# Kernel tuning notes

Measured on AMD Instinct MI355X. Metric: run time of the kernel, lower is better.

## Reference

```python
import jax, jax.numpy as jnp
import numpy as np

N, E = 20000, 160000
H, C1, C_OUT, D_IN = 4, 256, 512, 128
HID = H * C1  # 1024


def gat_conv(x, src, dst, W, a_src, a_dst, b, heads, ch, concat):
    n = x.shape[0]
    xw = (x @ W).reshape(n, heads, ch)                     # [N,H,C]
    es = jnp.sum(xw * a_src, axis=-1)                      # [N,H]
    ed = jnp.sum(xw * a_dst, axis=-1)                      # [N,H]
    e = jax.nn.leaky_relu(es[src] + ed[dst], 0.2)          # [Etot,H]
    m = jax.ops.segment_max(e, dst, num_segments=n)
    m = jnp.where(jnp.isfinite(m), m, 0.0)
    p = jnp.exp(e - m[dst])
    denom = jax.ops.segment_sum(p, dst, num_segments=n)
    alpha = p / (denom[dst] + 1e-16)                       # segment softmax
    out = jax.ops.segment_sum(alpha[:, :, None] * xw[src], dst, num_segments=n)
    out = out.reshape(n, heads * ch) if concat else out.mean(axis=1)
    return out + b


def layer_norm(x, g, b, eps=1e-5):
    mu = jnp.mean(x, axis=-1, keepdims=True)
    var = jnp.var(x, axis=-1, keepdims=True)
    return (x - mu) * jax.lax.rsqrt(var + eps) * g + b


def setup_inputs() -> dict:
    key = jax.random.key(0)
    ks = jax.random.split(key, 16)
    s1, s2, s3 = (2.0 / D_IN) ** 0.5, (2.0 / HID) ** 0.5, (2.0 / HID) ** 0.5
    return {
        "x": jax.random.normal(ks[0], (N, D_IN), jnp.float32),
        "edge_index": jax.random.randint(ks[1], (2, E), 0, N, jnp.int64),
        "W1": jax.random.normal(ks[2], (D_IN, H * C1), jnp.float32) * s1,
        "a_src1": jax.random.normal(ks[3], (H, C1), jnp.float32) * 0.1,
        "a_dst1": jax.random.normal(ks[4], (H, C1), jnp.float32) * 0.1,
        "b1": jnp.zeros((HID,), jnp.float32),
        "ln1_g": jnp.ones((HID,), jnp.float32),
        "ln1_b": jnp.zeros((HID,), jnp.float32),
        "W2": jax.random.normal(ks[5], (HID, H * C1), jnp.float32) * s2,
        "a_src2": jax.random.normal(ks[6], (H, C1), jnp.float32) * 0.1,
        "a_dst2": jax.random.normal(ks[7], (H, C1), jnp.float32) * 0.1,
        "b2": jnp.zeros((HID,), jnp.float32),
        "ln2_g": jnp.ones((HID,), jnp.float32),
        "ln2_b": jnp.zeros((HID,), jnp.float32),
        "W3": jax.random.normal(ks[8], (HID, C_OUT), jnp.float32) * s3,
        "a_src3": jax.random.normal(ks[9], (1, C_OUT), jnp.float32) * 0.1,
        "a_dst3": jax.random.normal(ks[10], (1, C_OUT), jnp.float32) * 0.1,
        "b3": jnp.zeros((C_OUT,), jnp.float32),
    }


def reference(x, edge_index, W1, a_src1, a_dst1, b1, ln1_g, ln1_b,
              W2, a_src2, a_dst2, b2, ln2_g, ln2_b,
              W3, a_src3, a_dst3, b3):
    # add self loops (PyG GATConv default add_self_loops=True)
    loops = jnp.arange(N, dtype=edge_index.dtype)
    src = jnp.concatenate([edge_index[0], loops])
    dst = jnp.concatenate([edge_index[1], loops])

    h = gat_conv(x, src, dst, W1, a_src1, a_dst1, b1, H, C1, True)
    h = jax.nn.elu(layer_norm(h, ln1_g, ln1_b))  # dropout: eval mode (identity)
    h = gat_conv(h, src, dst, W2, a_src2, a_dst2, b2, H, C1, True)
    h = jax.nn.elu(layer_norm(h, ln2_g, ln2_b))
    out = gat_conv(h, src, dst, W3, a_src3, a_dst3, b3, 1, C_OUT, True)
    return out
```

## Files before the change

kernel.cpp:

```cpp
#include <hip/hip_runtime.h>
#include <hip/hip_bf16.h>

typedef __hip_bfloat16 bf16;
typedef __attribute__((ext_vector_type(8))) short short8;
typedef __attribute__((ext_vector_type(4))) float float4v;

#define NN 20000
#define EE 160000
#define ET (NN + EE)

__device__ __forceinline__ float bf2f(bf16 v){ return __bfloat162float(v); }
__device__ __forceinline__ float raw2f(unsigned short u){ return __uint_as_float(((unsigned)u) << 16); }

struct Ptrs { const void* p[18]; int n[18]; };

__global__ void k_detect(Ptrs P, int* __restrict__ flags){
  int b = blockIdx.x;
  int t = threadIdx.x;
  if (b == 1){
    const int* e = (const int*)P.p[1];
    int odd = e[2*t + 1];
    unsigned long long m2 = __ballot(odd != 0);
    if (t == 0){ flags[1] = (m2 == 0ULL) ? 1 : 0; }
    return;
  }
  const unsigned* w = (const unsigned*)P.p[b];
  int nwords = P.n[b] / 2;
  unsigned v = w[t % nwords];
  int e8 = (v >> 7) & 0xFF;
  int looks = (e8 >= 100 && e8 <= 140) ? 1 : 0;
  unsigned long long mz = __ballot(v == 0u);
  unsigned long long ml = __ballot(looks);
  if (t == 0){
    int nz = __popcll(mz);
    int nonz = 64 - nz;
    int nl = __popcll(ml);
    flags[8+b] = (nonz > 0 && 2*nl >= nonz) ? 0 : 1;
  }
}

struct P13 { const void* src[13]; int off[13]; int n[13]; int fi[13]; };
struct PrepArgs {
  const void* xraw; bf16* Xc;
  const void* w1raw; bf16* Wt1;
  const void* w2raw; bf16* Wt2;
  const void* w3raw; bf16* Wt3;
  const int* eiraw; int* eic;
  P13 p13; float* prm;
  int* counts;
  const int* flags;
};

__device__ __forceinline__ void do_transpose(float (*tile)[33], const void* raw,
    bf16* wt, int K, int M, int f, int bx, int by, int t){
  int kb = by*32, mb = bx*32;
  int tx = t & 31, ty = t >> 5;
  for (int r = 0; r < 4; r++){
    int k = kb + ty + r*8;
    int m = mb + tx;
    float v = f ? ((const float*)raw)[(size_t)k*M+m] : bf2f(((const bf16*)raw)[(size_t)k*M+m]);
    tile[ty + r*8][tx] = v;
  }
  __syncthreads();
  for (int r = 0; r < 4; r++){
    int m = mb + ty + r*8;
    int k = kb + tx;
    wt[(size_t)m*K + k] = __float2bfloat16(tile[tx][ty + r*8]);
  }
}

__global__ __launch_bounds__(256) void k_prep(PrepArgs A){
  __shared__ float tile[32][33];
  int b = blockIdx.x, t = threadIdx.x;
  const int* flags = A.flags;
  if (b < 10000){
    int i = b*256 + t;
    if (flags[8+0]) A.Xc[i] = __float2bfloat16(((const float*)A.xraw)[i]);
    else            A.Xc[i] = ((const bf16*)A.xraw)[i];
  } else if (b < 10128){
    int r = b - 10000;
    do_transpose(tile, A.w1raw, A.Wt1, 128, 1024, flags[8+2], r & 31, r >> 5, t);
  } else if (b < 11152){
    int r = b - 10128;
    do_transpose(tile, A.w2raw, A.Wt2, 1024, 1024, flags[8+8], r & 31, r >> 5, t);
  } else if (b < 11664){
    int r = b - 11152;
    do_transpose(tile, A.w3raw, A.Wt3, 1024, 512, flags[8+14], r & 15, r >> 4, t);
  } else if (b < 12914){
    int i = (b - 11664)*256 + t;
    if (i < 2*EE) A.eic[i] = flags[1] ? A.eiraw[2*i] : A.eiraw[i];
  } else if (b < 12927){
    int pb = b - 12914;
    const void* s = A.p13.src[pb];
    int n = A.p13.n[pb];
    float* d = A.prm + A.p13.off[pb];
    int f = flags[8 + A.p13.fi[pb]];
    for (int i = t; i < n; i += 256)
      d[i] = f ? ((const float*)s)[i] : bf2f(((const bf16*)s)[i]);
  } else {
    int i = (b - 12927)*256 + t;
    if (i < NN) A.counts[i] = 1;
  }
}

__global__ void k_hist(const int* __restrict__ ei, int* __restrict__ counts){
  int e = blockIdx.x*256 + threadIdx.x;
  if (e < EE){
    int d = ei[EE + e];
    if (d >= 0 && d < NN) atomicAdd(&counts[d], 1);
  }
}

__global__ __launch_bounds__(1024) void k_scan(const int* __restrict__ counts, int* __restrict__ rp){
  __shared__ int wsum[16];
  __shared__ int sc;
  int t = threadIdx.x, lane = t & 63, wv = t >> 6;
  if (t == 0) sc = 0;
  __syncthreads();
  for (int base = 0; base < NN; base += 1024){
    int i = base + t;
    int v = (i < NN) ? counts[i] : 0;
    int x = v;
    #pragma unroll
    for (int o = 1; o < 64; o <<= 1){
      int y = __shfl_up(x, o, 64);
      if (lane >= o) x += y;
    }
    if (lane == 63) wsum[wv] = x;
    __syncthreads();
    if (wv == 0 && lane < 16){
      int w = wsum[lane];
      #pragma unroll
      for (int o = 1; o < 16; o <<= 1){
        int y = __shfl_up(w, o, 16);
        if ((lane & 15) >= o) w += y;
      }
      wsum[lane] = w;
    }
    __syncthreads();
    int carry = sc;
    int wpre = (wv > 0) ? wsum[wv-1] : 0;
    if (i < NN) rp[i] = carry + wpre + x - v;
    __syncthreads();
    if (t == 1023) sc = carry + wsum[15];
    __syncthreads();
  }
  if (t == 0) rp[NN] = sc;
}

__global__ void k_selfloop(const int* __restrict__ rp, int* __restrict__ cursor, int* __restrict__ col){
  int i = blockIdx.x*256 + threadIdx.x;
  if (i < NN){ int p = rp[i]; col[p] = i; cursor[i] = p + 1; }
}

__global__ void k_scatter(const int* __restrict__ ei, int* __restrict__ cursor, int* __restrict__ col){
  int e = blockIdx.x*256 + threadIdx.x;
  if (e < EE){
    int s = ei[e], d = ei[EE + e];
    if (d >= 0 && d < NN){
      int pos = atomicAdd(&cursor[d], 1);
      col[pos] = s;
    }
  }
}

__global__ void k_zero2(float* __restrict__ a, float* __restrict__ b, int n){
  int i = blockIdx.x*256 + threadIdx.x;
  if (i < n){ a[i] = 0.f; b[i] = 0.f; }
}

__global__ __launch_bounds__(256) void k_gemm_mfma(
    const bf16* __restrict__ X, const bf16* __restrict__ Wt, bf16* __restrict__ Y,
    const float* __restrict__ as_, const float* __restrict__ ad_,
    float* __restrict__ es, float* __restrict__ ed,
    int K, int M, int C, int H)
{
  __shared__ bf16 Xs[128*32];
  __shared__ bf16 Bs[128*32];
  int tid  = threadIdx.x;
  int wave = tid >> 6, lane = tid & 63;
  int quad = lane >> 4, l15 = lane & 15;
  int c0 = blockIdx.x * 128;
  int r0 = blockIdx.y * 128;
  int wr = (wave >> 1) * 64;
  int wc = (wave & 1) * 64;

  float4v acc[4][4];
  #pragma unroll
  for (int i=0;i<4;i++)
    #pragma unroll
    for (int j=0;j<4;j++)
      acc[i][j] = (float4v){0.f,0.f,0.f,0.f};

  for (int k0 = 0; k0 < K; k0 += 32){
    #pragma unroll
    for (int i = 0; i < 2; i++){
      int ch = i*256 + tid;
      int row = ch >> 2, kp = ch & 3;
      const bf16* gx = X  + (size_t)(r0 + row)*K + k0 + kp*8;
      const bf16* gb = Wt + (size_t)(c0 + row)*K + k0 + kp*8;
      __builtin_amdgcn_global_load_lds(
        (const __attribute__((address_space(1))) unsigned int*)gx,
        (__attribute__((address_space(3))) unsigned int*)(Xs + ch*8), 16, 0, 0);
      __builtin_amdgcn_global_load_lds(
        (const __attribute__((address_space(1))) unsigned int*)gb,
        (__attribute__((address_space(3))) unsigned int*)(Bs + ch*8), 16, 0, 0);
    }
    __syncthreads();

    short8 af[4], bfr[4];
    #pragma unroll
    for (int i = 0; i < 4; i++)
      af[i]  = *(const short8*)(Xs + ((size_t)(wr + i*16 + l15))*32 + quad*8);
    #pragma unroll
    for (int j = 0; j < 4; j++)
      bfr[j] = *(const short8*)(Bs + ((size_t)(wc + j*16 + l15))*32 + quad*8);
    #pragma unroll
    for (int i = 0; i < 4; i++)
      #pragma unroll
      for (int j = 0; j < 4; j++)
        acc[i][j] = __builtin_amdgcn_mfma_f32_16x16x32_bf16(af[i], bfr[j], acc[i][j], 0, 0, 0);
    __syncthreads();
  }

  int h = c0 / C;
  float asv[4], adv[4];
  #pragma unroll
  for (int j = 0; j < 4; j++){
    int colj = c0 + wc + j*16 + l15;
    asv[j] = as_[colj]; adv[j] = ad_[colj];
  }
  #pragma unroll
  for (int i = 0; i < 4; i++){
    int rbase = r0 + wr + i*16 + quad*4;
    #pragma unroll
    for (int rg = 0; rg < 4; rg++){
      int row = rbase + rg;
      bool ok = (row < NN);
      float pe = 0.f, pd = 0.f;
      #pragma unroll
      for (int j = 0; j < 4; j++){
        float v = acc[i][j][rg];
        int colj = c0 + wc + j*16 + l15;
        if (ok) Y[(size_t)row*M + colj] = __float2bfloat16(v);
        pe += v * asv[j];
        pd += v * adv[j];
      }
      #pragma unroll
      for (int o = 1; o < 16; o <<= 1){
        pe += __shfl_xor(pe, o, 64);
        pd += __shfl_xor(pd, o, 64);
      }
      if (ok && l15 == 0){
        atomicAdd(&es[row*H + h], pe);
        atomicAdd(&ed[row*H + h], pd);
      }
    }
  }
}

#define DCAP 1024
__global__ __launch_bounds__(256) void k_aggln(const int* __restrict__ rp, const int* __restrict__ col,
    const bf16* __restrict__ xw, const float* __restrict__ es, const float* __restrict__ ed,
    const float* __restrict__ bias, const float* __restrict__ gam, const float* __restrict__ bet,
    bf16* __restrict__ act){
  int n = blockIdx.x, t = threadIdx.x;
  int h = t >> 6;
  __shared__ float llog[DCAP][4];
  __shared__ int ssrc[DCAP];
  __shared__ float smv[4], srd[4];
  __shared__ float ls1[256], ls2[256];
  int e0 = rp[n], e1 = rp[n+1], deg = e1 - e0;
  float4 ed4 = *(const float4*)&ed[n*4];
  float a0=0.f, a1=0.f, a2=0.f, a3=0.f;

  if (deg <= DCAP){
    for (int j = t; j < deg; j += 256){
      int s = col[e0 + j];
      ssrc[j] = s;
      float4 e4 = *(const float4*)&es[s*4];
      float v0 = e4.x + ed4.x; llog[j][0] = v0 > 0.f ? v0 : 0.2f*v0;
      float v1 = e4.y + ed4.y; llog[j][1] = v1 > 0.f ? v1 : 0.2f*v1;
      float v2 = e4.z + ed4.z; llog[j][2] = v2 > 0.f ? v2 : 0.2f*v2;
      float v3 = e4.w + ed4.w; llog[j][3] = v3 > 0.f ? v3 : 0.2f*v3;
    }
    __syncthreads();
    if (t < 4){
      float m = -1e30f;
      for (int j = 0; j < deg; j++) m = fmaxf(m, llog[j][t]);
      float den = 0.f;
      for (int j = 0; j < deg; j++) den += __expf(llog[j][t] - m);
      smv[t] = m; srd[t] = 1.f/(den + 1e-16f);
    }
    __syncthreads();
    for (int j = t; j < deg; j += 256){
      #pragma unroll
      for (int hh = 0; hh < 4; hh++)
        llog[j][hh] = __expf(llog[j][hh] - smv[hh]) * srd[hh];
    }
    __syncthreads();
    for (int j = 0; j < deg; j++){
      int s = ssrc[j];
      float al = llog[j][h];
      ushort4 u = *(const ushort4*)((const unsigned short*)xw + (size_t)s*1024 + 4*t);
      a0 += al * raw2f(u.x);
      a1 += al * raw2f(u.y);
      a2 += al * raw2f(u.z);
      a3 += al * raw2f(u.w);
    }
  } else {
    if (t < 4){
      float m = -1e30f;
      for (int e = e0; e < e1; e++){
        float v = es[col[e]*4 + t] + ed[n*4 + t];
        v = v > 0.f ? v : 0.2f*v;
        m = fmaxf(m, v);
      }
      float den = 0.f;
      for (int e = e0; e < e1; e++){
        float v = es[col[e]*4 + t] + ed[n*4 + t];
        v = v > 0.f ? v : 0.2f*v;
        den += __expf(v - m);
      }
      smv[t] = m; srd[t] = 1.f/(den + 1e-16f);
    }
    __syncthreads();
    float edh = ed[n*4 + h];
    for (int e = e0; e < e1; e++){
      int s = col[e];
      float v = es[s*4 + h] + edh;
      v = v > 0.f ? v : 0.2f*v;
      float al = __expf(v - smv[h]) * srd[h];
      ushort4 u = *(const ushort4*)((const unsigned short*)xw + (size_t)s*1024 + 4*t);
      a0 += al * raw2f(u.x);
      a1 += al * raw2f(u.y);
      a2 += al * raw2f(u.z);
      a3 += al * raw2f(u.w);
    }
  }

  a0 += bias[4*t+0]; a1 += bias[4*t+1]; a2 += bias[4*t+2]; a3 += bias[4*t+3];
  float s1 = a0+a1+a2+a3;
  float s2 = a0*a0+a1*a1+a2*a2+a3*a3;
  ls1[t] = s1; ls2[t] = s2;
  __syncthreads();
  for (int o = 128; o > 0; o >>= 1){
    if (t < o){ ls1[t] += ls1[t+o]; ls2[t] += ls2[t+o]; }
    __syncthreads();
  }
  float mu  = ls1[0] * (1.f/1024.f);
  float var = ls2[0] * (1.f/1024.f) - mu*mu;
  float rstd = rsqrtf(fmaxf(var, 0.f) + 1e-5f);
  float v0 = (a0-mu)*rstd*gam[4*t+0] + bet[4*t+0];
  float v1 = (a1-mu)*rstd*gam[4*t+1] + bet[4*t+1];
  float v2 = (a2-mu)*rstd*gam[4*t+2] + bet[4*t+2];
  float v3 = (a3-mu)*rstd*gam[4*t+3] + bet[4*t+3];
  v0 = v0 > 0.f ? v0 : (__expf(v0)-1.f);
  v1 = v1 > 0.f ? v1 : (__expf(v1)-1.f);
  v2 = v2 > 0.f ? v2 : (__expf(v2)-1.f);
  v3 = v3 > 0.f ? v3 : (__expf(v3)-1.f);
  ushort4 o4;
  { bf16 hh2=__float2bfloat16(v0); o4.x=*(unsigned short*)&hh2; }
  { bf16 hh2=__float2bfloat16(v1); o4.y=*(unsigned short*)&hh2; }
  { bf16 hh2=__float2bfloat16(v2); o4.z=*(unsigned short*)&hh2; }
  { bf16 hh2=__float2bfloat16(v3); o4.w=*(unsigned short*)&hh2; }
  *(ushort4*)((unsigned short*)act + (size_t)n*1024 + 4*t) = o4;
}

__global__ __launch_bounds__(256) void k_agg3(const int* __restrict__ rp, const int* __restrict__ col,
    const bf16* __restrict__ xw, const float* __restrict__ es, const float* __restrict__ ed,
    const float* __restrict__ bias, float* __restrict__ out){
  int n = blockIdx.x, t = threadIdx.x;
  __shared__ float llog[DCAP];
  __shared__ int ssrc[DCAP];
  __shared__ float smv, srd;
  int e0 = rp[n], e1 = rp[n+1], deg = e1 - e0;
  float edv = ed[n];
  float a0 = 0.f, a1 = 0.f;

  if (deg <= DCAP){
    for (int j = t; j < deg; j += 256){
      int s = col[e0 + j];
      ssrc[j] = s;
      float v = es[s] + edv;
      llog[j] = v > 0.f ? v : 0.2f*v;
    }
    __syncthreads();
    if (t == 0){
      float m = -1e30f;
      for (int j = 0; j < deg; j++) m = fmaxf(m, llog[j]);
      float den = 0.f;
      for (int j = 0; j < deg; j++) den += __expf(llog[j] - m);
      smv = m; srd = 1.f/(den + 1e-16f);
    }
    __syncthreads();
    for (int j = t; j < deg; j += 256)
      llog[j] = __expf(llog[j] - smv) * srd;
    __syncthreads();
    for (int j = 0; j < deg; j++){
      int s = ssrc[j];
      float al = llog[j];
      ushort2 u = *(const ushort2*)((const unsigned short*)xw + (size_t)s*512 + 2*t);
      a0 += al * raw2f(u.x);
      a1 += al * raw2f(u.y);
    }
  } else {
    if (t == 0){
      float m = -1e30f;
      for (int e = e0; e < e1; e++){
        float v = es[col[e]] + edv;
        v = v > 0.f ? v : 0.2f*v;
        m = fmaxf(m, v);
      }
      float den = 0.f;
      for (int e = e0; e < e1; e++){
        float v = es[col[e]] + edv;
        v = v > 0.f ? v : 0.2f*v;
        den += __expf(v - m);
      }
      smv = m; srd = 1.f/(den + 1e-16f);
    }
    __syncthreads();
    for (int e = e0; e < e1; e++){
      int s = col[e];
      float v = es[s] + edv;
      v = v > 0.f ? v : 0.2f*v;
      float al = __expf(v - smv) * srd;
      ushort2 u = *(const ushort2*)((const unsigned short*)xw + (size_t)s*512 + 2*t);
      a0 += al * raw2f(u.x);
      a1 += al * raw2f(u.y);
    }
  }
  out[(size_t)n*512 + 2*t]     = a0 + bias[2*t];
  out[(size_t)n*512 + 2*t + 1] = a1 + bias[2*t+1];
}

__global__ void k_wssmall(float* __restrict__ out, float code){
  if (threadIdx.x == 0) out[0] = code;
}

extern "C" void kernel_launch(void* const* d_in, const int* in_sizes, int n_in,
                              void* d_out, int out_size, void* d_ws, size_t ws_size,
                              hipStream_t stream){
  float* out = (float*)d_out;
  char* ws = (char*)d_ws;

  static const int EXP_SZ[18] = {2560000, 320000, 131072, 1024,1024,1024,1024,1024,
                                 1048576, 1024,1024,1024,1024,1024,
                                 524288, 512,512,512};
  if (n_in != 18){ k_wssmall<<<1,64,0,stream>>>(out, 500.0f*301.0f); return; }
  for (int i = 0; i < 18; i++)
    if (in_sizes[i] != EXP_SZ[i]){ k_wssmall<<<1,64,0,stream>>>(out, 500.0f*302.0f); return; }
  if (out_size != NN*512){ k_wssmall<<<1,64,0,stream>>>(out, 500.0f*303.0f); return; }
  const size_t NEED = 93215360;
  if (ws_size < NEED){ k_wssmall<<<1,64,0,stream>>>(out, 500.0f*304.0f); return; }

  bf16* xw    = (bf16*) (ws);
  bf16* act   = (bf16*) (ws + 40960000);
  bf16* Xc    = (bf16*) (ws + 81920000);
  bf16* Wt1   = (bf16*) (ws + 87040000);
  bf16* Wt2   = (bf16*) (ws + 87302144);
  bf16* Wt3   = (bf16*) (ws + 89399296);
  float* prm  = (float*)(ws + 90447872);
  int*  flags = (int*)  (ws + 90494976);
  int*  eic   = (int*)  (ws + 90495232);
  float* es   = (float*)(ws + 91775232);
  int*  cur   = (int*)  (ws + 91775232);
  float* ed   = (float*)(ws + 92095232);
  int*  rp    = (int*)  (ws + 92415232);
  int*  col   = (int*)  (ws + 92495360);

  float *as1=prm+0, *ad1=prm+1024, *b1=prm+2048, *lg1=prm+3072, *lb1=prm+4096;
  float *as2=prm+5120, *ad2=prm+6144, *b2=prm+7168, *lg2=prm+8192, *lb2=prm+9216;
  float *as3=prm+10240, *ad3=prm+10752, *b3=prm+11264;

  const int TB = 256;
  int gbN = (NN + TB - 1)/TB;
  int gbE = (EE + TB - 1)/TB;

  {
    Ptrs P;
    for (int i=0;i<18;i++){ P.p[i]=d_in[i]; P.n[i]=in_sizes[i]; }
    k_detect<<<18, 64, 0, stream>>>(P, flags);
  }
  {
    PrepArgs A;
    A.xraw = d_in[0]; A.Xc = Xc;
    A.w1raw = d_in[2]; A.Wt1 = Wt1;
    A.w2raw = d_in[8]; A.Wt2 = Wt2;
    A.w3raw = d_in[14]; A.Wt3 = Wt3;
    A.eiraw = (const int*)d_in[1]; A.eic = eic;
    const int idx[13] = {3,4,5,6,7, 9,10,11,12,13, 15,16,17};
    const int off[13] = {0,1024,2048,3072,4096, 5120,6144,7168,8192,9216, 10240,10752,11264};
    const int nn [13] = {1024,1024,1024,1024,1024, 1024,1024,1024,1024,1024, 512,512,512};
    for (int i=0;i<13;i++){ A.p13.src[i]=d_in[idx[i]]; A.p13.off[i]=off[i]; A.p13.n[i]=nn[i]; A.p13.fi[i]=idx[i]; }
    A.prm = prm; A.counts = cur; A.flags = flags;
    k_prep<<<13006, TB, 0, stream>>>(A);
  }

  k_hist<<<gbE, TB, 0, stream>>>(eic, cur);
  k_scan<<<1, 1024, 0, stream>>>(cur, rp);
  k_selfloop<<<gbN, TB, 0, stream>>>(rp, cur, col);
  k_scatter<<<gbE, TB, 0, stream>>>(eic, cur, col);

  const int RB = (NN + 127)/128;
  dim3 g12(1024/128, RB);
  dim3 g3 (512/128,  RB);

  k_zero2<<<(NN*4+255)/256, TB, 0, stream>>>(es, ed, NN*4);
  k_gemm_mfma<<<g12, TB, 0, stream>>>(Xc, Wt1, xw, as1, ad1, es, ed, 128, 1024, 256, 4);
  k_aggln<<<NN, TB, 0, stream>>>(rp, col, xw, es, ed, b1, lg1, lb1, act);

  k_zero2<<<(NN*4+255)/256, TB, 0, stream>>>(es, ed, NN*4);
  k_gemm_mfma<<<g12, TB, 0, stream>>>(act, Wt2, xw, as2, ad2, es, ed, 1024, 1024, 256, 4);
  k_aggln<<<NN, TB, 0, stream>>>(rp, col, xw, es, ed, b2, lg2, lb2, act);

  k_zero2<<<(NN+255)/256, TB, 0, stream>>>(es, ed, NN);
  k_gemm_mfma<<<g3, TB, 0, stream>>>(act, Wt3, xw, as3, ad3, es, ed, 1024, 512, 512, 1);
  k_agg3<<<NN, TB, 0, stream>>>(rp, col, xw, es, ed, b3, out);
}
```

Measured before the change: 546.3 us.

## Remap GEMM blocks per XCD and unroll neighbor gather loops by four

The GEMM grid is padded to a multiple of eight row-blocks and block IDs are remapped so every column tile of a given row block lands on the same XCD. The intent is to let the row panel of X be reused through that XCD's L2. Separately, the aggregation loops in both the hidden-layer and output-layer kernels are unrolled by four, issuing four independent gather loads before accumulating so more memory requests are in flight. This adds some padded blocks that exit early and raises register pressure a little.

```diff
diff --git a/kernel.cpp b/kernel.cpp
--- a/kernel.cpp
+++ b/kernel.cpp
@@ -177,11 +177,19 @@
 {
   __shared__ bf16 Xs[128*32];
   __shared__ bf16 Bs[128*32];
+  int ncols = gridDim.x;
+  int bid = blockIdx.y * ncols + blockIdx.x;
+  int xcd  = bid & 7;
+  int rest = bid >> 3;
+  int colb = rest % ncols;
+  int rowb = xcd + 8 * (rest / ncols);
+  int r0 = rowb * 128;
+  if (r0 >= NN) return;
+  int c0 = colb * 128;
+
   int tid  = threadIdx.x;
   int wave = tid >> 6, lane = tid & 63;
   int quad = lane >> 4, l15 = lane & 15;
-  int c0 = blockIdx.x * 128;
-  int r0 = blockIdx.y * 128;
   int wr = (wave >> 1) * 64;
   int wc = (wave & 1) * 64;
 
@@ -273,6 +281,7 @@
   int e0 = rp[n], e1 = rp[n+1], deg = e1 - e0;
   float4 ed4 = *(const float4*)&ed[n*4];
   float a0=0.f, a1=0.f, a2=0.f, a3=0.f;
+  const unsigned short* xwu = (const unsigned short*)xw;
 
   if (deg <= DCAP){
     for (int j = t; j < deg; j += 256){
@@ -299,14 +308,24 @@
         llog[j][hh] = __expf(llog[j][hh] - smv[hh]) * srd[hh];
     }
     __syncthreads();
-    for (int j = 0; j < deg; j++){
+    int j = 0;
+    for (; j + 4 <= deg; j += 4){
+      int s0=ssrc[j], s1=ssrc[j+1], s2=ssrc[j+2], s3=ssrc[j+3];
+      float al0=llog[j][h], al1=llog[j+1][h], al2=llog[j+2][h], al3=llog[j+3][h];
+      ushort4 u0 = *(const ushort4*)(xwu + (size_t)s0*1024 + 4*t);
+      ushort4 u1 = *(const ushort4*)(xwu + (size_t)s1*1024 + 4*t);
+      ushort4 u2 = *(const ushort4*)(xwu + (size_t)s2*1024 + 4*t);
+      ushort4 u3 = *(const ushort4*)(xwu + (size_t)s3*1024 + 4*t);
+      a0 += al0*raw2f(u0.x); a1 += al0*raw2f(u0.y); a2 += al0*raw2f(u0.z); a3 += al0*raw2f(u0.w);
+      a0 += al1*raw2f(u1.x); a1 += al1*raw2f(u1.y); a2 += al1*raw2f(u1.z); a3 += al1*raw2f(u1.w);
+      a0 += al2*raw2f(u2.x); a1 += al2*raw2f(u2.y); a2 += al2*raw2f(u2.z); a3 += al2*raw2f(u2.w);
+      a0 += al3*raw2f(u3.x); a1 += al3*raw2f(u3.y); a2 += al3*raw2f(u3.z); a3 += al3*raw2f(u3.w);
+    }
+    for (; j < deg; j++){
       int s = ssrc[j];
       float al = llog[j][h];
-      ushort4 u = *(const ushort4*)((const unsigned short*)xw + (size_t)s*1024 + 4*t);
-      a0 += al * raw2f(u.x);
-      a1 += al * raw2f(u.y);
-      a2 += al * raw2f(u.z);
-      a3 += al * raw2f(u.w);
+      ushort4 u = *(const ushort4*)(xwu + (size_t)s*1024 + 4*t);
+      a0 += al*raw2f(u.x); a1 += al*raw2f(u.y); a2 += al*raw2f(u.z); a3 += al*raw2f(u.w);
     }
   } else {
     if (t < 4){
@@ -331,11 +350,8 @@
       float v = es[s*4 + h] + edh;
       v = v > 0.f ? v : 0.2f*v;
       float al = __expf(v - smv[h]) * srd[h];
-      ushort4 u = *(const ushort4*)((const unsigned short*)xw + (size_t)s*1024 + 4*t);
-      a0 += al * raw2f(u.x);
-      a1 += al * raw2f(u.y);
-      a2 += al * raw2f(u.z);
-      a3 += al * raw2f(u.w);
+      ushort4 u = *(const ushort4*)(xwu + (size_t)s*1024 + 4*t);
+      a0 += al*raw2f(u.x); a1 += al*raw2f(u.y); a2 += al*raw2f(u.z); a3 += al*raw2f(u.w);
     }
   }
 
@@ -377,6 +393,7 @@
   int e0 = rp[n], e1 = rp[n+1], deg = e1 - e0;
   float edv = ed[n];
   float a0 = 0.f, a1 = 0.f;
+  const unsigned short* xwu = (const unsigned short*)xw;
 
   if (deg <= DCAP){
     for (int j = t; j < deg; j += 256){
@@ -397,12 +414,24 @@
     for (int j = t; j < deg; j += 256)
       llog[j] = __expf(llog[j] - smv) * srd;
     __syncthreads();
-    for (int j = 0; j < deg; j++){
+    int j = 0;
+    for (; j + 4 <= deg; j += 4){
+      int s0=ssrc[j], s1=ssrc[j+1], s2=ssrc[j+2], s3=ssrc[j+3];
+      float al0=llog[j], al1=llog[j+1], al2=llog[j+2], al3=llog[j+3];
+      ushort2 u0 = *(const ushort2*)(xwu + (size_t)s0*512 + 2*t);
+      ushort2 u1 = *(const ushort2*)(xwu + (size_t)s1*512 + 2*t);
+      ushort2 u2 = *(const ushort2*)(xwu + (size_t)s2*512 + 2*t);
+      ushort2 u3 = *(const ushort2*)(xwu + (size_t)s3*512 + 2*t);
+      a0 += al0*raw2f(u0.x); a1 += al0*raw2f(u0.y);
+      a0 += al1*raw2f(u1.x); a1 += al1*raw2f(u1.y);
+      a0 += al2*raw2f(u2.x); a1 += al2*raw2f(u2.y);
+      a0 += al3*raw2f(u3.x); a1 += al3*raw2f(u3.y);
+    }
+    for (; j < deg; j++){
       int s = ssrc[j];
       float al = llog[j];
-      ushort2 u = *(const ushort2*)((const unsigned short*)xw + (size_t)s*512 + 2*t);
-      a0 += al * raw2f(u.x);
-      a1 += al * raw2f(u.y);
+      ushort2 u = *(const ushort2*)(xwu + (size_t)s*512 + 2*t);
+      a0 += al*raw2f(u.x); a1 += al*raw2f(u.y);
     }
   } else {
     if (t == 0){
@@ -426,9 +455,8 @@
       float v = es[s] + edv;
       v = v > 0.f ? v : 0.2f*v;
       float al = __expf(v - smv) * srd;
-      ushort2 u = *(const ushort2*)((const unsigned short*)xw + (size_t)s*512 + 2*t);
-      a0 += al * raw2f(u.x);
-      a1 += al * raw2f(u.y);
+      ushort2 u = *(const ushort2*)(xwu + (size_t)s*512 + 2*t);
+      a0 += al*raw2f(u.x); a1 += al*raw2f(u.y);
     }
   }
   out[(size_t)n*512 + 2*t]     = a0 + bias[2*t];
@@ -504,8 +532,9 @@
   k_scatter<<<gbE, TB, 0, stream>>>(eic, cur, col);
 
   const int RB = (NN + 127)/128;
-  dim3 g12(1024/128, RB);
-  dim3 g3 (512/128,  RB);
+  const int R8 = ((RB + 7)/8)*8;
+  dim3 g12(1024/128, R8);
+  dim3 g3 (512/128,  R8);
 
   k_zero2<<<(NN*4+255)/256, TB, 0, stream>>>(es, ed, NN*4);
   k_gemm_mfma<<<g12, TB, 0, stream>>>(Xc, Wt1, xw, as1, ad1, es, ed, 128, 1024, 256, 4);
```

Measured after the change: 542.8 us. Within noise of the previous version (-0.6%).
